# Performance work log

Measured on AMD Instinct MI355X. Metric: run time of the kernel, lower is better.

Reference implementation:

```python
import jax, jax.numpy as jnp
import numpy as np
from jax.scipy.special import gammaln

BIG_NEG = -1e9
MAX_K = 20  # args.sm_max_span_length


def setup_inputs() -> dict:
    key = jax.random.key(0)
    ks = jax.random.split(key, 7)
    B, N, d, C = 16, 2048, 256, 128
    features = jax.random.normal(ks[0], (B, N, d), dtype=jnp.float32)
    lengths = jax.random.randint(ks[1], (B,), N // 2, N + 1)
    gaussian_means = jax.random.normal(ks[2], (C, d), dtype=jnp.float32)
    cov_diag = jax.random.uniform(ks[3], (d,), minval=0.5, maxval=1.5, dtype=jnp.float32)
    transition_logits = jax.random.normal(ks[4], (C, C), dtype=jnp.float32)
    init_logits = jax.random.uniform(ks[5], (C,), dtype=jnp.float32)
    poisson_log_rates = jax.random.normal(ks[6], (C,), dtype=jnp.float32) * 0.5 + 1.5
    return {"features": features, "lengths": lengths, "gaussian_means": gaussian_means,
            "cov_diag": cov_diag, "transition_logits": transition_logits,
            "init_logits": init_logits, "poisson_log_rates": poisson_log_rates}


def _emission_log_probs(features, means, cov_diag):
    # Diagonal-covariance MultivariateNormal log-prob, one class per column.
    # Quadratic form expanded to avoid materializing [B,N,C,d].
    inv_var = 1.0 / cov_diag
    d = features.shape[-1]
    const = -0.5 * (d * jnp.log(2.0 * jnp.pi) + jnp.sum(jnp.log(cov_diag)))
    xq = jnp.einsum('bnd,d->bn', features * features, inv_var)          # [B,N]
    mq = jnp.einsum('cd,d->c', means * means, inv_var)                  # [C]
    xm = jnp.einsum('bnd,cd->bnc', features, means * inv_var)           # [B,N,C]
    return const - 0.5 * (xq[..., None] + mq[None, None, :] - 2.0 * xm)  # [B,N,C]


def _length_log_probs(log_rates, K):
    # Poisson log-prob for span lengths k = 1..K.
    ks = jnp.arange(1, K + 1, dtype=jnp.float32)[:, None]               # [K,1]
    return ks * log_rates[None, :] - jnp.exp(log_rates)[None, :] - gammaln(ks + 1.0)  # [K,C]


def _transition_log_probs(transition_logits):
    C = transition_logits.shape[0]
    masked = jnp.where(jnp.eye(C, dtype=bool), BIG_NEG, transition_logits)  # no self-transitions
    return jax.nn.log_softmax(masked, axis=0)  # normalized over destination class (dim 0)


def _semimarkov_logZ(emis_lp, lengths, init_lp, trans_lp, len_lp, K):
    # Segmental (semi-Markov) CRF forward algorithm with sliding-window span sums.
    B, N, C = emis_lp.shape
    cum = jnp.concatenate([jnp.zeros((B, 1, C), emis_lp.dtype), jnp.cumsum(emis_lp, axis=1)], axis=1)
    cum_pad = jnp.concatenate([jnp.zeros((B, K, C), emis_lp.dtype), cum], axis=1)  # idx t+K <-> position t
    beta0 = jnp.full((B, N + 1 + K, C), BIG_NEG, emis_lp.dtype)
    beta0 = beta0.at[:, K, :].set(init_lp[None, :])  # position 0: initial distribution
    len_rev = len_lp[::-1]  # len_rev[j] == length log-prob of span length K-j

    def step(beta, t):
        w = jax.lax.dynamic_slice(beta, (0, t, 0), (B, K, C))        # beta at positions t-K..t-1
        cw = jax.lax.dynamic_slice(cum_pad, (0, t, 0), (B, K, C))
        ct = jax.lax.dynamic_slice(cum_pad, (0, t + K, 0), (B, 1, C))
        span = w + len_rev[None, :, :] + (ct - cw)                    # [B,K,C] span scores ending at t
        alpha_t = jax.nn.logsumexp(span, axis=1)                      # [B,C]
        beta_t = jax.nn.logsumexp(alpha_t[:, None, :] + trans_lp[None, :, :], axis=2)  # to-class
        beta = jax.lax.dynamic_update_slice(beta, beta_t[:, None, :], (0, t + K, 0))
        return beta, alpha_t

    _, alphas = jax.lax.scan(step, beta0, jnp.arange(1, N + 1))       # alphas: [N,B,C]
    final = alphas[lengths - 1, jnp.arange(B)]                        # [B,C] at each sequence end
    return jax.nn.logsumexp(final, axis=1)                            # [B] log partition


def reference(features, lengths, gaussian_means, cov_diag, transition_logits, init_logits, poisson_log_rates):
    emis_lp = _emission_log_probs(features, gaussian_means, cov_diag)
    init_lp = jax.nn.log_softmax(init_logits, axis=0)
    trans_lp = _transition_log_probs(transition_logits)
    len_lp = _length_log_probs(poisson_log_rates, MAX_K)
    return _semimarkov_logZ(emis_lp, lengths, init_lp, trans_lp, len_lp, MAX_K)
```

## Files before the change

kernel.cpp:

```cpp
#include <hip/hip_runtime.h>
#include <math.h>

#define Bb 16
#define Nn 2048
#define Dd 256
#define Cc 128
#define Kk 20
#define BIG_NEG -1.0e9f

#define WS_EMIS   0
#define WS_MSC    (WS_EMIS + Bb*Nn*Cc)
#define WS_XQ     (WS_MSC + Cc*Dd)
#define WS_ECHAN  (WS_XQ + Bb*Nn)
#define WS_T      (WS_ECHAN + Cc)
#define WS_LEN    (WS_T + Cc*Cc)
#define WS_INIT   (WS_LEN + Kk*Cc)
#define WS_IVAR   (WS_INIT + Cc)

typedef __attribute__((ext_vector_type(8))) short short8;
typedef __attribute__((ext_vector_type(4))) float float4v;

__device__ __forceinline__ unsigned short f32_to_bf16(float x) {
  unsigned int u = __builtin_bit_cast(unsigned int, x);
  u = (u + 0x7FFFu + ((u >> 16) & 1u)) >> 16;
  return (unsigned short)u;
}

#define DPP_STEP(x, op, ctrl, rmask)                                          \
  do {                                                                        \
    int _yi = __builtin_amdgcn_update_dpp(                                    \
        __builtin_bit_cast(int, x), __builtin_bit_cast(int, x), ctrl, rmask,  \
        0xF, true);                                                           \
    x = op(x, __builtin_bit_cast(float, _yi));                                \
  } while (0)

__device__ __forceinline__ float dpp_add(float a, float b) { return a + b; }

__device__ __forceinline__ float wave_max64(float x) {
  DPP_STEP(x, fmaxf, 0xB1, 0xF);
  DPP_STEP(x, fmaxf, 0x4E, 0xF);
  DPP_STEP(x, fmaxf, 0x141, 0xF);
  DPP_STEP(x, fmaxf, 0x140, 0xF);
  DPP_STEP(x, fmaxf, 0x142, 0xA);
  DPP_STEP(x, fmaxf, 0x143, 0xC);
  return __builtin_bit_cast(float,
      __builtin_amdgcn_readlane(__builtin_bit_cast(int, x), 63));
}

__device__ __forceinline__ float wave_sum64(float x) {
  DPP_STEP(x, dpp_add, 0xB1, 0xF);
  DPP_STEP(x, dpp_add, 0x4E, 0xF);
  DPP_STEP(x, dpp_add, 0x141, 0xF);
  DPP_STEP(x, dpp_add, 0x140, 0xF);
  DPP_STEP(x, dpp_add, 0x142, 0xA);
  DPP_STEP(x, dpp_add, 0x143, 0xC);
  return __builtin_bit_cast(float,
      __builtin_amdgcn_readlane(__builtin_bit_cast(int, x), 63));
}

__global__ void prep_kernel(const float* __restrict__ means,
                            const float* __restrict__ cov,
                            const float* __restrict__ tl,
                            const float* __restrict__ il,
                            const float* __restrict__ plr,
                            float* __restrict__ ws) {
  __shared__ float s_iv[Dd];
  __shared__ float s_red[4];
  __shared__ float s_tlse[Cc];
  int tid = threadIdx.x;

  float cv = cov[tid];
  float iv = 1.0f / cv;
  s_iv[tid] = iv;
  ws[WS_IVAR + tid] = iv;
  float lg = __logf(cv);
  #pragma unroll
  for (int off = 1; off < 64; off <<= 1) lg += __shfl_xor(lg, off, 64);
  if ((tid & 63) == 0) s_red[tid >> 6] = lg;
  __syncthreads();
  float logdet = s_red[0] + s_red[1] + s_red[2] + s_red[3];
  float cconst = -0.5f * ((float)Dd * 1.8378770664093453f + logdet);

  unsigned short* mscb = (unsigned short*)(ws + WS_MSC);
  for (int idx = tid; idx < Cc * Dd; idx += 256) {
    int d = idx & (Dd - 1);
    mscb[idx] = f32_to_bf16(means[idx] * s_iv[d]);
  }
  if (tid < Cc) {
    float acc = 0.0f;
    for (int d = 0; d < Dd; d++) {
      float m = means[tid * Dd + d];
      acc = fmaf(m * m, s_iv[d], acc);
    }
    ws[WS_ECHAN + tid] = cconst - 0.5f * acc;
  }
  for (int idx = tid; idx < Kk * Cc; idx += 256) {
    int L = idx / Cc + 1;
    int c = idx & (Cc - 1);
    float r = plr[c];
    ws[WS_LEN + idx] = (float)L * r - __expf(r) - lgammaf((float)(L + 1));
  }

  __syncthreads();
  float x = (tid < Cc) ? il[tid] : -INFINITY;
  float mx = x;
  #pragma unroll
  for (int off = 1; off < 64; off <<= 1) mx = fmaxf(mx, __shfl_xor(mx, off, 64));
  if ((tid & 63) == 0) s_red[tid >> 6] = mx;
  __syncthreads();
  float M = fmaxf(s_red[0], s_red[1]);
  float se = (tid < Cc) ? __expf(x - M) : 0.0f;
  #pragma unroll
  for (int off = 1; off < 64; off <<= 1) se += __shfl_xor(se, off, 64);
  __syncthreads();
  if ((tid & 63) == 0) s_red[tid >> 6] = se;
  __syncthreads();
  float lse = M + __logf(s_red[0] + s_red[1]);
  if (tid < Cc) ws[WS_INIT + tid] = x - lse;

  if (tid < Cc) {
    int j = tid;
    float m2 = -INFINITY;
    for (int i = 0; i < Cc; i++) if (i != j) m2 = fmaxf(m2, tl[i * Cc + j]);
    float s2 = 0.0f;
    for (int i = 0; i < Cc; i++) if (i != j) s2 += __expf(tl[i * Cc + j] - m2);
    s_tlse[j] = m2 + __logf(s2);
  }
  __syncthreads();
  for (int idx = tid; idx < Cc * Cc; idx += 256) {
    int i = idx / Cc;
    int j = idx & (Cc - 1);
    ws[WS_T + idx] = (i == j) ? 0.0f : __expf(tl[idx] - s_tlse[j]);
  }
}

__global__ void xq_kernel(const float* __restrict__ f, float* __restrict__ ws) {
  int pos = blockIdx.x * 4 + (threadIdx.x >> 6);
  int lane = threadIdx.x & 63;
  const float4 fv = *(const float4*)&f[(size_t)pos * Dd + lane * 4];
  const float4 vv = *(const float4*)&ws[WS_IVAR + lane * 4];
  float a = fv.x * fv.x * vv.x + fv.y * fv.y * vv.y +
            fv.z * fv.z * vv.z + fv.w * fv.w * vv.w;
  #pragma unroll
  for (int off = 1; off < 64; off <<= 1) a += __shfl_xor(a, off, 64);
  if (lane == 0) ws[WS_XQ + pos] = a;
}

__launch_bounds__(256)
__global__ void emis_mfma_kernel(const float* __restrict__ f, float* __restrict__ ws) {
  const unsigned short* msc = (const unsigned short*)(ws + WS_MSC);
  float* emis = ws + WS_EMIS;
  int tid = threadIdx.x;
  int w = tid >> 6, lane = tid & 63, g = lane >> 4, l16 = lane & 15;
  int b = blockIdx.x >> 6;
  int n0 = (blockIdx.x & 63) << 5;
  int c0 = w << 5;

  const float* fbase = f + (size_t)(b * Nn + n0) * Dd;
  float4v acc[2][2];
  #pragma unroll
  for (int rt = 0; rt < 2; rt++)
    #pragma unroll
    for (int ct = 0; ct < 2; ct++) acc[rt][ct] = (float4v){0.f, 0.f, 0.f, 0.f};

  #pragma unroll
  for (int k0 = 0; k0 < Dd; k0 += 32) {
    int kk = k0 + g * 8;
    short8 afr[2], bfr[2];
    #pragma unroll
    for (int rt = 0; rt < 2; rt++) {
      const float* src = fbase + (size_t)(rt * 16 + l16) * Dd + kk;
      float4 v0 = *(const float4*)src;
      float4 v1 = *(const float4*)(src + 4);
      short8 fr;
      fr[0] = (short)f32_to_bf16(v0.x); fr[1] = (short)f32_to_bf16(v0.y);
      fr[2] = (short)f32_to_bf16(v0.z); fr[3] = (short)f32_to_bf16(v0.w);
      fr[4] = (short)f32_to_bf16(v1.x); fr[5] = (short)f32_to_bf16(v1.y);
      fr[6] = (short)f32_to_bf16(v1.z); fr[7] = (short)f32_to_bf16(v1.w);
      afr[rt] = fr;
    }
    #pragma unroll
    for (int ct = 0; ct < 2; ct++)
      bfr[ct] = *(const short8*)&msc[(size_t)(c0 + ct * 16 + l16) * Dd + kk];
    #pragma unroll
    for (int rt = 0; rt < 2; rt++)
      #pragma unroll
      for (int ct = 0; ct < 2; ct++)
        acc[rt][ct] = __builtin_amdgcn_mfma_f32_16x16x32_bf16(afr[rt], bfr[ct], acc[rt][ct], 0, 0, 0);
  }

  #pragma unroll
  for (int rt = 0; rt < 2; rt++) {
    #pragma unroll
    for (int ct = 0; ct < 2; ct++) {
      int cc = c0 + ct * 16 + l16;
      float ec = ws[WS_ECHAN + cc];
      #pragma unroll
      for (int r = 0; r < 4; r++) {
        int row = rt * 16 + g * 4 + r;
        int nn = n0 + row;
        emis[(size_t)(b * Nn + nn) * Cc + cc] =
            ec - 0.5f * ws[WS_XQ + b * Nn + nn] + acc[rt][ct][r];
      }
    }
  }
}

__launch_bounds__(128, 1)
__global__ void scan_kernel(const int* __restrict__ lengths,
                            const float* __restrict__ ws,
                            float* __restrict__ out) {
  __shared__ __align__(16) unsigned short lds_pb[2][Cc];
  __shared__ float lds_wmax[2][2];
  __shared__ float lds_ps[2];
  int tid = threadIdx.x;
  int b = blockIdx.x;
  int c = tid;
  int w = tid >> 6;
  int lane = tid & 63;
  int g = lane >> 4;
  int len_b = lengths[b];
  const float* emis = ws + WS_EMIS + (size_t)b * Nn * Cc;

  short8 Tf[4][4];
  {
    const float* T = ws + WS_T;
    int row_lo = w * 64 + (lane & 15);
    int kg = g * 8;
    #pragma unroll
    for (int nt = 0; nt < 4; nt++)
      #pragma unroll
      for (int kt = 0; kt < 4; kt++) {
        const float* src = &T[(size_t)(row_lo + nt * 16) * Cc + kt * 32 + kg];
        short8 fr;
        #pragma unroll
        for (int j = 0; j < 8; j++) fr[j] = (short)f32_to_bf16(src[j]);
        Tf[nt][kt] = fr;
      }
  }

  float lenv[Kk];
  #pragma unroll
  for (int i = 0; i < Kk; i++) lenv[i] = ws[WS_LEN + i * Cc + c];
  float len0 = lenv[0];
  float dlen[Kk - 1];
  #pragma unroll
  for (int i = 1; i < Kk; i++) dlen[i - 1] = lenv[i] - lenv[i - 1];

  float h[Kk];
  #pragma unroll
  for (int i = 0; i < Kk; i++) h[i] = BIG_NEG;

  float gnew = ws[WS_INIT + c];
  float pm = BIG_NEG;
  float ps = 19.0f;

  float cum = emis[0 * Cc + c];
  float e[8], en[8];
  #pragma unroll
  for (int i = 0; i < 8; i++) e[i] = emis[(size_t)(1 + i) * Cc + c];

  bool done = false;
  for (int tg = 1; tg <= Nn && !done; tg += 8) {
    #pragma unroll
    for (int i = 0; i < 8; i++) {
      int t = tg + i;
      int buf = t & 1;

      float h0 = gnew + len0;
      float m = fmaxf(pm, h0);
      float sfix = fmaf(ps, __expf(pm - m), __expf(h0 - m));
      float mabs = m + cum;
      float wm = wave_max64(mabs);
      float p = sfix * __expf(mabs - wm);
      lds_pb[buf][c] = f32_to_bf16(p);
      if (lane == 0) lds_wmax[buf][w] = wm;
      bool is_out = (t == len_b);
      if (is_out) {
        float pssum = wave_sum64(p);
        if (lane == 0) lds_ps[w] = pssum;
      }
      h[0] = h0;
      __syncthreads();

      if (i == 0) {
        #pragma unroll
        for (int j = 0; j < 8; j++) {
          int r = tg + 8 + j; if (r > Nn - 1) r = Nn - 1;
          en[j] = emis[(size_t)r * Cc + c];
        }
      }
      float MA = lds_wmax[buf][0], MB = lds_wmax[buf][1];
      const unsigned short* pb = lds_pb[buf];
      short8 pa[4];
      #pragma unroll
      for (int kt = 0; kt < 4; kt++)
        pa[kt] = *(const short8*)&pb[kt * 32 + g * 8];

      #pragma unroll
      for (int k = Kk - 1; k > 0; k--) h[k] = h[k - 1] + dlen[k - 1];
      float m2[10];
      #pragma unroll
      for (int k = 0; k < 9; k++) m2[k] = fmaxf(h[1 + 2 * k], h[2 + 2 * k]);
      m2[9] = h[19];
      float m4a = fmaxf(fmaxf(m2[0], m2[1]), fmaxf(m2[2], m2[3]));
      float m4b = fmaxf(fmaxf(m2[4], m2[5]), fmaxf(m2[6], m2[7]));
      float pm2 = fmaxf(fmaxf(m4a, m4b), fmaxf(m2[8], m2[9]));
      float ex[Kk - 1];
      #pragma unroll
      for (int k = 1; k < Kk; k++) ex[k - 1] = __expf(h[k] - pm2);
      float s4[5];
      s4[0] = (ex[0] + ex[1]) + (ex[2] + ex[3]);
      s4[1] = (ex[4] + ex[5]) + (ex[6] + ex[7]);
      s4[2] = (ex[8] + ex[9]) + (ex[10] + ex[11]);
      s4[3] = (ex[12] + ex[13]) + (ex[14] + ex[15]);
      s4[4] = (ex[16] + ex[17]) + ex[18];
      float ps2 = ((s4[0] + s4[1]) + (s4[2] + s4[3])) + s4[4];

      float4v z = {0.0f, 0.0f, 0.0f, 0.0f};
      float4v accA[4], accB[4];
      #pragma unroll
      for (int nt = 0; nt < 4; nt++) {
        accA[nt] = __builtin_amdgcn_mfma_f32_16x16x32_bf16(pa[1], Tf[nt][1],
                     __builtin_amdgcn_mfma_f32_16x16x32_bf16(pa[0], Tf[nt][0], z, 0, 0, 0),
                     0, 0, 0);
        accB[nt] = __builtin_amdgcn_mfma_f32_16x16x32_bf16(pa[3], Tf[nt][3],
                     __builtin_amdgcn_mfma_f32_16x16x32_bf16(pa[2], Tf[nt][2], z, 0, 0, 0),
                     0, 0, 0);
      }
      float Mt = fmaxf(MA, MB);
      float sA = __expf(MA - Mt), sB = __expf(MB - Mt);
      float qa0 = (g == 0) ? accA[0][0] : accA[1][0];
      float qa1 = (g == 2) ? accA[2][0] : accA[3][0];
      float qa = (g < 2) ? qa0 : qa1;
      float qb0 = (g == 0) ? accB[0][0] : accB[1][0];
      float qb1 = (g == 2) ? accB[2][0] : accB[3][0];
      float qb = (g < 2) ? qb0 : qb1;
      float q = qa * sA + qb * sB;

      float rel = cum - Mt;
      gnew = (q > 0.0f) ? (__logf(q) - rel) : (-80.0f - rel);

      if (is_out) {
        if (tid == 0) out[b] = Mt + __logf(lds_ps[0] * sA + lds_ps[1] * sB);
        done = true;
        break;
      }
      pm = pm2;
      ps = ps2;
      cum += e[i];
    }
    if (!done) {
      #pragma unroll
      for (int i = 0; i < 8; i++) e[i] = en[i];
    }
  }
}

extern "C" void kernel_launch(void* const* d_in, const int* in_sizes, int n_in,
                              void* d_out, int out_size, void* d_ws, size_t ws_size,
                              hipStream_t stream) {
  const float* features = (const float*)d_in[0];
  const int* lengths = (const int*)d_in[1];
  const float* means = (const float*)d_in[2];
  const float* cov = (const float*)d_in[3];
  const float* tl = (const float*)d_in[4];
  const float* il = (const float*)d_in[5];
  const float* plr = (const float*)d_in[6];
  float* out = (float*)d_out;
  float* ws = (float*)d_ws;

  prep_kernel<<<1, 256, 0, stream>>>(means, cov, tl, il, plr, ws);
  xq_kernel<<<(Bb * Nn) / 4, 256, 0, stream>>>(features, ws);
  emis_mfma_kernel<<<Bb * (Nn / 32), 256, 0, stream>>>(features, ws);
  scan_kernel<<<Bb, 128, 0, stream>>>(lengths, ws, out);
}
```

Baseline: 1.541 ms.

## Rewrite semi-Markov scan as single-wave fp8 MFMA recurrence in log2 domain

The scan kernel now runs one 64-lane wave per sequence, with each lane owning two classes. This removes the cross-wave __syncthreads and LDS max exchange from every timestep. The transition matvec uses a single scaled 16x16x128 fp8 MFMA per output tile instead of chained bf16 MFMAs. The span window is kept as a multiplicative running vector using exp2, and emissions, lengths and init are prescaled by log2e so the inner loop uses native exp2/log2. The trade is lower precision from fp8 transition and probability operands, plus a different numerical recurrence that risks accuracy drift over long sequences.

Result: no change. 1.551 ms (+0.7%).

```diff
diff --git a/kernel.cpp b/kernel.cpp
--- a/kernel.cpp
+++ b/kernel.cpp
@@ -7,6 +7,8 @@
 #define Cc 128
 #define Kk 20
 #define BIG_NEG -1.0e9f
+#define LOG2E 1.4426950408889634f
+#define LN2   0.6931471805599453f
 
 #define WS_EMIS   0
 #define WS_MSC    (WS_EMIS + Bb*Nn*Cc)
@@ -19,6 +21,7 @@
 
 typedef __attribute__((ext_vector_type(8))) short short8;
 typedef __attribute__((ext_vector_type(4))) float float4v;
+typedef __attribute__((ext_vector_type(8))) int int8v;
 
 __device__ __forceinline__ unsigned short f32_to_bf16(float x) {
   unsigned int u = __builtin_bit_cast(unsigned int, x);
@@ -56,6 +59,10 @@
   DPP_STEP(x, dpp_add, 0x143, 0xC);
   return __builtin_bit_cast(float,
       __builtin_amdgcn_readlane(__builtin_bit_cast(int, x), 63));
+}
+
+__device__ __forceinline__ int chan_of_k(int kpos) {
+  return (kpos & 1) ? (64 + (kpos >> 1)) : (kpos >> 1);
 }
 
 __global__ void prep_kernel(const float* __restrict__ means,
@@ -98,7 +105,7 @@
     int L = idx / Cc + 1;
     int c = idx & (Cc - 1);
     float r = plr[c];
-    ws[WS_LEN + idx] = (float)L * r - __expf(r) - lgammaf((float)(L + 1));
+    ws[WS_LEN + idx] = ((float)L * r - __expf(r) - lgammaf((float)(L + 1))) * LOG2E;
   }
 
   __syncthreads();
@@ -116,7 +123,7 @@
   if ((tid & 63) == 0) s_red[tid >> 6] = se;
   __syncthreads();
   float lse = M + __logf(s_red[0] + s_red[1]);
-  if (tid < Cc) ws[WS_INIT + tid] = x - lse;
+  if (tid < Cc) ws[WS_INIT + tid] = (x - lse) * LOG2E;
 
   if (tid < Cc) {
     int j = tid;
@@ -200,159 +207,167 @@
         int row = rt * 16 + g * 4 + r;
         int nn = n0 + row;
         emis[(size_t)(b * Nn + nn) * Cc + cc] =
-            ec - 0.5f * ws[WS_XQ + b * Nn + nn] + acc[rt][ct][r];
-      }
-    }
-  }
-}
-
-__launch_bounds__(128, 1)
+            (ec - 0.5f * ws[WS_XQ + b * Nn + nn] + acc[rt][ct][r]) * LOG2E;
+      }
+    }
+  }
+}
+
+__launch_bounds__(64, 1)
 __global__ void scan_kernel(const int* __restrict__ lengths,
                             const float* __restrict__ ws,
                             float* __restrict__ out) {
-  __shared__ __align__(16) unsigned short lds_pb[2][Cc];
-  __shared__ float lds_wmax[2][2];
-  __shared__ float lds_ps[2];
-  int tid = threadIdx.x;
+  __shared__ unsigned short s_p[64];
+  int lane = threadIdx.x;
+  int lg4 = lane >> 4, n16 = lane & 15;
   int b = blockIdx.x;
-  int c = tid;
-  int w = tid >> 6;
-  int lane = tid & 63;
-  int g = lane >> 4;
   int len_b = lengths[b];
   const float* emis = ws + WS_EMIS + (size_t)b * Nn * Cc;
-
-  short8 Tf[4][4];
+  const int sc1 = 0x7F7F7F7F;
+
+  int8v Tf[8];
   {
     const float* T = ws + WS_T;
-    int row_lo = w * 64 + (lane & 15);
-    int kg = g * 8;
-    #pragma unroll
-    for (int nt = 0; nt < 4; nt++)
-      #pragma unroll
-      for (int kt = 0; kt < 4; kt++) {
-        const float* src = &T[(size_t)(row_lo + nt * 16) * Cc + kt * 32 + kg];
-        short8 fr;
-        #pragma unroll
-        for (int j = 0; j < 8; j++) fr[j] = (short)f32_to_bf16(src[j]);
-        Tf[nt][kt] = fr;
-      }
-  }
-
-  float lenv[Kk];
-  #pragma unroll
-  for (int i = 0; i < Kk; i++) lenv[i] = ws[WS_LEN + i * Cc + c];
-  float len0 = lenv[0];
-  float dlen[Kk - 1];
-  #pragma unroll
-  for (int i = 1; i < Kk; i++) dlen[i - 1] = lenv[i] - lenv[i - 1];
-
-  float h[Kk];
-  #pragma unroll
-  for (int i = 0; i < Kk; i++) h[i] = BIG_NEG;
-
-  float gnew = ws[WS_INIT + c];
-  float pm = BIG_NEG;
-  float ps = 19.0f;
-
-  float cum = emis[0 * Cc + c];
-  float e[8], en[8];
-  #pragma unroll
-  for (int i = 0; i < 8; i++) e[i] = emis[(size_t)(1 + i) * Cc + c];
+    #pragma unroll
+    for (int nt = 0; nt < 8; nt++) {
+      const float* Trow = &T[(size_t)(nt * 16 + n16) * Cc];
+      #pragma unroll
+      for (int dw = 0; dw < 8; dw++) {
+        int kbase = lg4 * 32 + dw * 4;
+        float t0 = 64.0f * Trow[chan_of_k(kbase + 0)];
+        float t1 = 64.0f * Trow[chan_of_k(kbase + 1)];
+        float t2 = 64.0f * Trow[chan_of_k(kbase + 2)];
+        float t3 = 64.0f * Trow[chan_of_k(kbase + 3)];
+        int d = __builtin_amdgcn_cvt_pk_fp8_f32(t0, t1, 0, false);
+        d = __builtin_amdgcn_cvt_pk_fp8_f32(t2, t3, d, true);
+        Tf[nt][dw] = d;
+      }
+    }
+  }
+
+  int cidx[2] = {lane, lane + 64};
+  float len0[2], E2[2][Kk - 1];
+  #pragma unroll
+  for (int ch = 0; ch < 2; ch++) {
+    float lenv[Kk];
+    #pragma unroll
+    for (int k = 0; k < Kk; k++) lenv[k] = ws[WS_LEN + k * Cc + cidx[ch]];
+    len0[ch] = lenv[0];
+    #pragma unroll
+    for (int k = 0; k < Kk - 1; k++)
+      E2[ch][k] = __builtin_amdgcn_exp2f(lenv[k + 1] - lenv[k]);
+  }
+
+  float wv[2][Kk - 1];
+  #pragma unroll
+  for (int ch = 0; ch < 2; ch++)
+    #pragma unroll
+    for (int j = 0; j < Kk - 1; j++) wv[ch][j] = 0.0f;
+  float a[2] = {0.0f, 0.0f};
+  float L19[2] = {-1.0e30f, -1.0e30f};
+  float gnew[2], cum[2];
+  gnew[0] = ws[WS_INIT + lane];
+  gnew[1] = ws[WS_INIT + lane + 64];
+  cum[0] = emis[0 * Cc + lane];
+  cum[1] = emis[0 * Cc + lane + 64];
+
+  float e[2][8], en[2][8];
+  #pragma unroll
+  for (int i = 0; i < 8; i++) {
+    e[0][i] = emis[(size_t)(1 + i) * Cc + lane];
+    e[1][i] = emis[(size_t)(1 + i) * Cc + lane + 64];
+  }
 
   bool done = false;
   for (int tg = 1; tg <= Nn && !done; tg += 8) {
     #pragma unroll
     for (int i = 0; i < 8; i++) {
       int t = tg + i;
-      int buf = t & 1;
-
-      float h0 = gnew + len0;
-      float m = fmaxf(pm, h0);
-      float sfix = fmaf(ps, __expf(pm - m), __expf(h0 - m));
-      float mabs = m + cum;
-      float wm = wave_max64(mabs);
-      float p = sfix * __expf(mabs - wm);
-      lds_pb[buf][c] = f32_to_bf16(p);
-      if (lane == 0) lds_wmax[buf][w] = wm;
+      {
+        int r = tg + 8 + i; if (r > Nn - 1) r = Nn - 1;
+        en[0][i] = emis[(size_t)r * Cc + lane];
+        en[1][i] = emis[(size_t)r * Cc + lane + 64];
+      }
+
+      float h0[2], mm[2], eh[2], sfix[2], mab[2];
+      #pragma unroll
+      for (int ch = 0; ch < 2; ch++) {
+        h0[ch] = gnew[ch] + len0[ch];
+        mm[ch] = fmaxf(L19[ch], h0[ch]);
+        float eL = __builtin_amdgcn_exp2f(L19[ch] - mm[ch]);
+        eh[ch] = __builtin_amdgcn_exp2f(h0[ch] - mm[ch]);
+        sfix[ch] = eL + eh[ch];
+        mab[ch] = mm[ch] + cum[ch];
+      }
+      float lmax = fmaxf(mab[0], mab[1]);
+      float wm = wave_max64(lmax);
+      float p0 = sfix[0] * __builtin_amdgcn_exp2f(mab[0] - wm);
+      float p1 = sfix[1] * __builtin_amdgcn_exp2f(mab[1] - wm);
+      int pk = __builtin_amdgcn_cvt_pk_fp8_f32(p0, p1, 0, false);
+      s_p[lane] = (unsigned short)pk;
       bool is_out = (t == len_b);
+
+      const int4* ap = (const int4*)((const char*)s_p + lg4 * 32);
+      int4 ra = ap[0];
+      int4 rb = ap[1];
+      int8v A;
+      A[0] = ra.x; A[1] = ra.y; A[2] = ra.z; A[3] = ra.w;
+      A[4] = rb.x; A[5] = rb.y; A[6] = rb.z; A[7] = rb.w;
+
+      float4v D0, D1, D2, D3, D4, D5, D6, D7;
+      {
+        float4v z = {0.0f, 0.0f, 0.0f, 0.0f};
+        D0 = __builtin_amdgcn_mfma_scale_f32_16x16x128_f8f6f4(A, Tf[0], z, 0, 0, 0, sc1, 0, sc1);
+        D1 = __builtin_amdgcn_mfma_scale_f32_16x16x128_f8f6f4(A, Tf[1], z, 0, 0, 0, sc1, 0, sc1);
+        D2 = __builtin_amdgcn_mfma_scale_f32_16x16x128_f8f6f4(A, Tf[2], z, 0, 0, 0, sc1, 0, sc1);
+        D3 = __builtin_amdgcn_mfma_scale_f32_16x16x128_f8f6f4(A, Tf[3], z, 0, 0, 0, sc1, 0, sc1);
+        D4 = __builtin_amdgcn_mfma_scale_f32_16x16x128_f8f6f4(A, Tf[4], z, 0, 0, 0, sc1, 0, sc1);
+        D5 = __builtin_amdgcn_mfma_scale_f32_16x16x128_f8f6f4(A, Tf[5], z, 0, 0, 0, sc1, 0, sc1);
+        D6 = __builtin_amdgcn_mfma_scale_f32_16x16x128_f8f6f4(A, Tf[6], z, 0, 0, 0, sc1, 0, sc1);
+        D7 = __builtin_amdgcn_mfma_scale_f32_16x16x128_f8f6f4(A, Tf[7], z, 0, 0, 0, sc1, 0, sc1);
+      }
+
+      float S19n[2];
+      #pragma unroll
+      for (int ch = 0; ch < 2; ch++) {
+        float phi = __builtin_amdgcn_exp2f(a[ch] - mm[ch]);
+        #pragma unroll
+        for (int j = Kk - 2; j >= 1; j--)
+          wv[ch][j] = wv[ch][j - 1] * (E2[ch][j] * phi);
+        wv[ch][0] = eh[ch] * E2[ch][0];
+        float s4[5];
+        s4[0] = (wv[ch][0] + wv[ch][1]) + (wv[ch][2] + wv[ch][3]);
+        s4[1] = (wv[ch][4] + wv[ch][5]) + (wv[ch][6] + wv[ch][7]);
+        s4[2] = (wv[ch][8] + wv[ch][9]) + (wv[ch][10] + wv[ch][11]);
+        s4[3] = (wv[ch][12] + wv[ch][13]) + (wv[ch][14] + wv[ch][15]);
+        s4[4] = (wv[ch][16] + wv[ch][17]) + wv[ch][18];
+        S19n[ch] = ((s4[0] + s4[1]) + (s4[2] + s4[3])) + s4[4];
+      }
+
+      float q0 = (lg4 == 0) ? D0[0] : (lg4 == 1) ? D1[0] : (lg4 == 2) ? D2[0] : D3[0];
+      float q1 = (lg4 == 0) ? D4[0] : (lg4 == 1) ? D5[0] : (lg4 == 2) ? D6[0] : D7[0];
+      float rel0 = cum[0] - wm;
+      float rel1 = cum[1] - wm;
+      gnew[0] = (q0 > 0.0f) ? (__builtin_amdgcn_logf(q0) - 6.0f - rel0) : BIG_NEG;
+      gnew[1] = (q1 > 0.0f) ? (__builtin_amdgcn_logf(q1) - 6.0f - rel1) : BIG_NEG;
+
       if (is_out) {
-        float pssum = wave_sum64(p);
-        if (lane == 0) lds_ps[w] = pssum;
-      }
-      h[0] = h0;
-      __syncthreads();
-
-      if (i == 0) {
-        #pragma unroll
-        for (int j = 0; j < 8; j++) {
-          int r = tg + 8 + j; if (r > Nn - 1) r = Nn - 1;
-          en[j] = emis[(size_t)r * Cc + c];
-        }
-      }
-      float MA = lds_wmax[buf][0], MB = lds_wmax[buf][1];
-      const unsigned short* pb = lds_pb[buf];
-      short8 pa[4];
-      #pragma unroll
-      for (int kt = 0; kt < 4; kt++)
-        pa[kt] = *(const short8*)&pb[kt * 32 + g * 8];
-
-      #pragma unroll
-      for (int k = Kk - 1; k > 0; k--) h[k] = h[k - 1] + dlen[k - 1];
-      float m2[10];
-      #pragma unroll
-      for (int k = 0; k < 9; k++) m2[k] = fmaxf(h[1 + 2 * k], h[2 + 2 * k]);
-      m2[9] = h[19];
-      float m4a = fmaxf(fmaxf(m2[0], m2[1]), fmaxf(m2[2], m2[3]));
-      float m4b = fmaxf(fmaxf(m2[4], m2[5]), fmaxf(m2[6], m2[7]));
-      float pm2 = fmaxf(fmaxf(m4a, m4b), fmaxf(m2[8], m2[9]));
-      float ex[Kk - 1];
-      #pragma unroll
-      for (int k = 1; k < Kk; k++) ex[k - 1] = __expf(h[k] - pm2);
-      float s4[5];
-      s4[0] = (ex[0] + ex[1]) + (ex[2] + ex[3]);
-      s4[1] = (ex[4] + ex[5]) + (ex[6] + ex[7]);
-      s4[2] = (ex[8] + ex[9]) + (ex[10] + ex[11]);
-      s4[3] = (ex[12] + ex[13]) + (ex[14] + ex[15]);
-      s4[4] = (ex[16] + ex[17]) + ex[18];
-      float ps2 = ((s4[0] + s4[1]) + (s4[2] + s4[3])) + s4[4];
-
-      float4v z = {0.0f, 0.0f, 0.0f, 0.0f};
-      float4v accA[4], accB[4];
-      #pragma unroll
-      for (int nt = 0; nt < 4; nt++) {
-        accA[nt] = __builtin_amdgcn_mfma_f32_16x16x32_bf16(pa[1], Tf[nt][1],
-                     __builtin_amdgcn_mfma_f32_16x16x32_bf16(pa[0], Tf[nt][0], z, 0, 0, 0),
-                     0, 0, 0);
-        accB[nt] = __builtin_amdgcn_mfma_f32_16x16x32_bf16(pa[3], Tf[nt][3],
-                     __builtin_amdgcn_mfma_f32_16x16x32_bf16(pa[2], Tf[nt][2], z, 0, 0, 0),
-                     0, 0, 0);
-      }
-      float Mt = fmaxf(MA, MB);
-      float sA = __expf(MA - Mt), sB = __expf(MB - Mt);
-      float qa0 = (g == 0) ? accA[0][0] : accA[1][0];
-      float qa1 = (g == 2) ? accA[2][0] : accA[3][0];
-      float qa = (g < 2) ? qa0 : qa1;
-      float qb0 = (g == 0) ? accB[0][0] : accB[1][0];
-      float qb1 = (g == 2) ? accB[2][0] : accB[3][0];
-      float qb = (g < 2) ? qb0 : qb1;
-      float q = qa * sA + qb * sB;
-
-      float rel = cum - Mt;
-      gnew = (q > 0.0f) ? (__logf(q) - rel) : (-80.0f - rel);
-
-      if (is_out) {
-        if (tid == 0) out[b] = Mt + __logf(lds_ps[0] * sA + lds_ps[1] * sB);
+        float psum = wave_sum64(p0 + p1);
+        if (lane == 0) out[b] = LN2 * (wm + __builtin_amdgcn_logf(psum));
         done = true;
         break;
       }
-      pm = pm2;
-      ps = ps2;
-      cum += e[i];
+
+      #pragma unroll
+      for (int ch = 0; ch < 2; ch++) {
+        a[ch] = mm[ch];
+        L19[ch] = mm[ch] + __builtin_amdgcn_logf(S19n[ch]);
+        cum[ch] += e[ch][i];
+      }
     }
     if (!done) {
       #pragma unroll
-      for (int i = 0; i < 8; i++) e[i] = en[i];
+      for (int i = 0; i < 8; i++) { e[0][i] = en[0][i]; e[1][i] = en[1][i]; }
     }
   }
 }
@@ -373,5 +388,5 @@
   prep_kernel<<<1, 256, 0, stream>>>(means, cov, tl, il, plr, ws);
   xq_kernel<<<(Bb * Nn) / 4, 256, 0, stream>>>(features, ws);
   emis_mfma_kernel<<<Bb * (Nn / 32), 256, 0, stream>>>(features, ws);
-  scan_kernel<<<Bb, 128, 0, stream>>>(lengths, ws, out);
-}
+  scan_kernel<<<Bb, 64, 0, stream>>>(lengths, ws, out);
+}
```
